# Kernel optimization log

Hardware: AMD Instinct MI355X
Metric: run time of the kernel (lower is better)

The kernel has to match this reference:

```python
import jax, jax.numpy as jnp
import numpy as np

H = 8          # num_attention_heads
HEAD_DIM = 24  # 192 / 8


def setup_inputs() -> dict:
    key = jax.random.key(0)
    k1, k2, k3 = jax.random.split(key, 3)
    B, S, D = 4, 2048, 192
    x = jax.random.normal(k1, (B, S, D), dtype=jnp.float32)
    mask0 = jnp.zeros((B, 1, 1, S), dtype=jnp.float32)  # HF additive attention mask
    w_attn = jax.random.normal(k2, (D, 3 * D), dtype=jnp.float32) * 0.02
    b_attn = jnp.zeros((3 * D,), dtype=jnp.float32)
    w_proj = jax.random.normal(k3, (D, D), dtype=jnp.float32) * 0.02
    b_proj = jnp.zeros((D,), dtype=jnp.float32)
    return {"x": x, "mask0": mask0, "w_attn": w_attn, "b_attn": b_attn,
            "w_proj": w_proj, "b_proj": b_proj}


def reference(x, mask0, w_attn, b_attn, w_proj, b_proj):
    B, S, D = x.shape
    # fused QKV projection (GPT2 Conv1D: x @ W + b)
    qkv = x @ w_attn + b_attn                       # [B,S,3D]
    q, k, v = jnp.split(qkv, 3, axis=-1)
    def split_heads(t):
        return t.reshape(B, S, H, HEAD_DIM).transpose(0, 2, 1, 3)  # [B,H,S,hd]
    q, k, v = split_heads(q), split_heads(k), split_heads(v)
    # scaled QK^T
    scores = jnp.einsum('bhqd,bhkd->bhqk', q, k) / jnp.sqrt(
        jnp.asarray(HEAD_DIM, dtype=q.dtype))
    # causal mask (masked_fill with dtype min), then additive padding mask
    causal = jnp.tril(jnp.ones((S, S), dtype=bool))
    mask_value = jnp.finfo(scores.dtype).min
    scores = jnp.where(causal, scores, mask_value) + mask0
    attn = jax.nn.softmax(scores, axis=-1)          # [B,H,S,S]
    # attn_dropout is identity in eval mode
    out = jnp.einsum('bhqk,bhkd->bhqd', attn, v)    # [B,H,S,hd]
    out = out.transpose(0, 2, 1, 3).reshape(B, S, D)
    return out @ w_proj + b_proj
```

## Files before the change

### kernel.cpp

```cpp
#include <hip/hip_runtime.h>

typedef unsigned short u16;
typedef unsigned int u32;
typedef __bf16 bf16x8 __attribute__((ext_vector_type(8)));
typedef float f32x4 __attribute__((ext_vector_type(4)));
typedef float f32x16 __attribute__((ext_vector_type(16)));
typedef u32 u32x2 __attribute__((ext_vector_type(2)));
typedef u32 u32x4 __attribute__((ext_vector_type(4)));

#define NB 4
#define NS 2048
#define ND 192
#define NH 8
#define HD 24
#define NM (NB*NS)
#define N3 (3*ND)
#define NBH (NB*NH)

#define LOG2E 1.4426950408889634f
#define QSCALE (0.20412414523193152f * 1.4426950408889634f)

__device__ __forceinline__ u16 f2bf(float f){
  union { float f; unsigned u; } a; a.f = f;
  unsigned r = a.u + 0x7fffu + ((a.u >> 16) & 1u);
  return (u16)(r >> 16);
}
__device__ __forceinline__ u32 cvtpk(float lo, float hi){
  u32 r; asm("v_cvt_pk_bf16_f32 %0, %1, %2" : "=v"(r) : "v"(lo), "v"(hi)); return r;
}
__device__ __forceinline__ void pswap(u32 &a, u32 &b){
  asm("v_permlane32_swap_b32 %0, %1" : "+v"(a), "+v"(b));
}

__device__ __forceinline__ void transpose64(
    const float* __restrict__ src, int srcN, u16* __restrict__ dst, int dstK,
    int k0, int n0, u16 (*sh)[68], int tid)
{
  int r = tid >> 2, cs = tid & 3;
  const float* sp = src + (size_t)(k0 + r)*srcN + n0 + cs*16;
  #pragma unroll
  for (int q = 0; q < 4; ++q) {
    float4 v = *(const float4*)(sp + q*4);
    u16 o[4] = { f2bf(v.x), f2bf(v.y), f2bf(v.z), f2bf(v.w) };
    *(u32x2*)&sh[r][cs*16 + q*4] = *(const u32x2*)o;
  }
  __syncthreads();
  int n = tid >> 2, ks = tid & 3;
  u16 tmp[16];
  #pragma unroll
  for (int j = 0; j < 16; ++j) tmp[j] = sh[ks*16 + j][n];
  u16* dp = dst + (size_t)(n0 + n)*dstK + k0 + ks*16;
  *(u32x4*)dp       = *(const u32x4*)tmp;
  *(u32x4*)(dp + 8) = *(const u32x4*)(tmp + 8);
}

__global__ __launch_bounds__(256) void prep_kernel(
    const float* __restrict__ x, const float* __restrict__ w_attn,
    const float* __restrict__ w_proj,
    u16* __restrict__ xb, u16* __restrict__ wta, u16* __restrict__ wtp)
{
  __shared__ u16 sh[64][68];
  const int bid = blockIdx.x, tid = threadIdx.x;
  if (bid < 1536) {
    int i = bid*256 + tid;
    float4 v = reinterpret_cast<const float4*>(x)[i];
    u16 o[4] = { f2bf(v.x), f2bf(v.y), f2bf(v.z), f2bf(v.w) };
    *reinterpret_cast<u32x2*>(xb + (size_t)i*4) = *(const u32x2*)o;
  } else if (bid < 1536 + 27) {
    int t = bid - 1536; int kt = t/9, nt = t%9;
    transpose64(w_attn, N3, wta, ND, kt*64, nt*64, sh, tid);
  } else {
    int t = bid - 1563; int kt = t/3, nt = t%3;
    transpose64(w_proj, ND, wtp, ND, kt*64, nt*64, sh, tid);
  }
}

__global__ __launch_bounds__(256) void qkv_kernel(
    const u16* __restrict__ xb, const u16* __restrict__ wta,
    const float* __restrict__ b_attn, const float* __restrict__ mask0,
    u16* __restrict__ qp, u16* __restrict__ kp, u16* __restrict__ vtp)
{
  __shared__ u16 tile[96*72];
  const int m0 = blockIdx.x*64, n0 = blockIdx.y*96;
  const int tid = threadIdx.x;
  const int w = tid >> 6, lane = tid & 63, c = lane & 15, g = lane >> 4;
  f32x4 acc[6] = {};
  const int ar = m0 + w*16 + c;
  #pragma unroll
  for (int ks = 0; ks < 6; ++ks) {
    bf16x8 af = *(const bf16x8*)(xb + (size_t)ar*ND + ks*32 + g*8);
    #pragma unroll
    for (int t = 0; t < 6; ++t) {
      bf16x8 bfr = *(const bf16x8*)(wta + (size_t)(n0 + t*16 + c)*ND + ks*32 + g*8);
      acc[t] = __builtin_amdgcn_mfma_f32_16x16x32_bf16(af, bfr, acc[t], 0, 0, 0);
    }
  }
  const int b = m0 >> 11, sb = m0 & (NS-1);
  if (n0 >= 384) {
    const int h0 = (n0 - 384)/HD;
    #pragma unroll
    for (int t = 0; t < 6; ++t) {
      float bias = b_attn[n0 + t*16 + c];
      #pragma unroll
      for (int r = 0; r < 4; ++r)
        tile[(t*16 + c)*72 + w*16 + g*4 + r] = f2bf(acc[t][r] + bias);
    }
    __syncthreads();
    if (tid < 200) {
      int row = tid >> 1, seg = tid & 1;
      if (row < 96) {
        int hl = row / HD, dv = row % HD;
        u16* dst = vtp + ((size_t)((b*NH + h0 + hl)*32 + dv))*NS + sb + seg*32;
        const u16* src = &tile[row*72 + seg*32];
        #pragma unroll
        for (int q = 0; q < 4; ++q)
          *(u32x4*)(dst + q*8) = *(const u32x4*)(src + q*8);
      } else {
        int hl = row - 96;
        u16* dst = vtp + ((size_t)((b*NH + h0 + hl)*32 + 24))*NS + sb + seg*32;
        u16 ones[8] = {0x3F80,0x3F80,0x3F80,0x3F80,0x3F80,0x3F80,0x3F80,0x3F80};
        #pragma unroll
        for (int q = 0; q < 4; ++q)
          *(u32x4*)(dst + q*8) = *(const u32x4*)ones;
      }
    }
  } else {
    const bool isQ = (n0 < 192);
    const float scl = isQ ? QSCALE : 1.0f;
    #pragma unroll
    for (int t = 0; t < 6; ++t) {
      float bias = b_attn[n0 + t*16 + c];
      #pragma unroll
      for (int r = 0; r < 4; ++r)
        tile[(w*16 + g*4 + r)*104 + t*16 + c] = f2bf((acc[t][r] + bias)*scl);
    }
    __syncthreads();
    int row = tid >> 2, run = tid & 3;
    int h0 = (n0 % 192)/HD;
    u16 d24 = isQ ? (u16)0x3F80
                  : f2bf(mask0[b*NS + sb + row] * LOG2E);
    const u16* src = &tile[row*104 + run*24];
    union { u32x4 q[4]; u16 s[32]; } buf;
    buf.q[0] = *(const u32x4*)(src);
    buf.q[1] = *(const u32x4*)(src + 8);
    buf.q[2] = *(const u32x4*)(src + 16);
    buf.s[24] = d24;
    #pragma unroll
    for (int j = 25; j < 32; ++j) buf.s[j] = 0;
    u16* dst = (isQ ? qp : kp)
             + ((size_t)((b*NS + sb + row)*NH + h0 + run))*32;
    #pragma unroll
    for (int q = 0; q < 4; ++q)
      *(u32x4*)(dst + q*8) = buf.q[q];
  }
}

__global__ __launch_bounds__(256) void attn_kernel(
    const u16* __restrict__ qp, const u16* __restrict__ kp,
    const u16* __restrict__ vtp, u16* __restrict__ ao)
{
  __shared__ u16 klds[2][64][40];
  __shared__ u16 vlds[2][32][72];
  u16 (*ot)[32][40] = (u16(*)[32][40])klds;

  const int bh = blockIdx.x;
  const int g  = 15 - (int)blockIdx.y;
  const int b = bh >> 3, h = bh & 7;
  const int tid = threadIdx.x;
  const int w = tid >> 6, lane = tid & 63, c = lane & 31, hi = lane >> 5;
  const int q0 = g*128 + w*32;
  const int nt = 2*g + 2;

  const size_t rowstride = NH*32;
  const size_t qkbase = (size_t)b*NS*rowstride + h*32;

  const u16* qrow = qp + qkbase + (size_t)(q0 + c)*rowstride;
  bf16x8 qf0 = *(const bf16x8*)(qrow + hi*8);
  bf16x8 qf1 = *(const bf16x8*)(qrow + 16 + hi*8);

  const int krow = tid >> 2, kch = tid & 3;
  const int vrow = tid >> 3, vch = tid & 7;
  const u16* kgsrc = kp + qkbase + (size_t)krow*rowstride + kch*8;
  const u16* vgsrc = vtp + ((size_t)(bh*32 + vrow))*NS + vch*8;

  u32x4 kreg = *(const u32x4*)(kgsrc);
  u32x4 vreg = *(const u32x4*)(vgsrc);
  *(u32x4*)&klds[0][krow][kch*8] = kreg;
  *(u32x4*)&vlds[0][vrow][vch*8] = vreg;
  __syncthreads();

  f32x16 o = {0};
  const f32x16 z16 = {0};
  float m = 0.f;

  for (int t = 0; t < nt; ++t) {
    const int cur = t & 1;
    if (t + 1 < nt) {
      kreg = *(const u32x4*)(kgsrc + (size_t)(t+1)*64*rowstride);
      vreg = *(const u32x4*)(vgsrc + (t+1)*64);
    }
    const int kb0 = t*64;
    if (kb0 <= q0) {
      const bool a1 = (kb0 + 32 <= q0);
      bf16x8 ka0 = *(const bf16x8*)&klds[cur][c][hi*8];
      bf16x8 ka1 = *(const bf16x8*)&klds[cur][c][16 + hi*8];
      f32x16 st = __builtin_amdgcn_mfma_f32_32x32x16_bf16(ka0, qf0, z16, 0, 0, 0);
      st        = __builtin_amdgcn_mfma_f32_32x32x16_bf16(ka1, qf1, st,  0, 0, 0);
      f32x16 su;
      if (a1) {
        bf16x8 kb0f = *(const bf16x8*)&klds[cur][32 + c][hi*8];
        bf16x8 kb1f = *(const bf16x8*)&klds[cur][32 + c][16 + hi*8];
        su = __builtin_amdgcn_mfma_f32_32x32x16_bf16(kb0f, qf0, z16, 0, 0, 0);
        su = __builtin_amdgcn_mfma_f32_32x32x16_bf16(kb1f, qf1, su,  0, 0, 0);
      }
      float pm = -3.0e38f;
      if (kb0 == q0) {
        #pragma unroll
        for (int r = 0; r < 16; ++r) {
          int krel = (r & 3) + 8*(r >> 2) + 4*hi;
          float s = (krel > c) ? -3.0e38f : st[r];
          st[r] = s; pm = fmaxf(pm, s);
        }
      } else {
        #pragma unroll
        for (int r = 0; r < 16; ++r) pm = fmaxf(pm, st[r]);
      }
      if (a1) {
        if (kb0 + 32 == q0) {
          #pragma unroll
          for (int r = 0; r < 16; ++r) {
            int krel = (r & 3) + 8*(r >> 2) + 4*hi;
            float s = (krel > c) ? -3.0e38f : su[r];
            su[r] = s; pm = fmaxf(pm, s);
          }
        } else {
          #pragma unroll
          for (int r = 0; r < 16; ++r) pm = fmaxf(pm, su[r]);
        }
      }
      if (!__all(pm - m <= 8.f)) {
        float pm2 = fmaxf(pm, __shfl_xor(pm, 32));
        float mn = fmaxf(m, pm2);
        float al = __builtin_amdgcn_exp2f(m - mn);
        #pragma unroll
        for (int r = 0; r < 16; ++r) o[r] *= al;
        m = mn;
      }
      #pragma unroll
      for (int r = 0; r < 16; ++r) st[r] = __builtin_amdgcn_exp2f(st[r] - m);
      if (a1) {
        #pragma unroll
        for (int r = 0; r < 16; ++r) su[r] = __builtin_amdgcn_exp2f(su[r] - m);
      }
      {
        u32 a0 = cvtpk(st[0], st[1]),  b0 = cvtpk(st[4], st[5]);
        u32 a1w = cvtpk(st[2], st[3]), b1 = cvtpk(st[6], st[7]);
        pswap(a0, b0); pswap(a1w, b1);
        u32 a2 = cvtpk(st[8], st[9]),  b2 = cvtpk(st[12], st[13]);
        u32 a3 = cvtpk(st[10], st[11]), b3 = cvtpk(st[14], st[15]);
        pswap(a2, b2); pswap(a3, b3);
        union { u32 wrd[4]; bf16x8 v; } pf0, pf1;
        pf0.wrd[0] = a0; pf0.wrd[1] = a1w; pf0.wrd[2] = b0; pf0.wrd[3] = b1;
        pf1.wrd[0] = a2; pf1.wrd[1] = a3;  pf1.wrd[2] = b2; pf1.wrd[3] = b3;
        bf16x8 va0 = *(const bf16x8*)&vlds[cur][c][hi*8];
        bf16x8 va1 = *(const bf16x8*)&vlds[cur][c][16 + hi*8];
        o = __builtin_amdgcn_mfma_f32_32x32x16_bf16(va0, pf0.v, o, 0, 0, 0);
        o = __builtin_amdgcn_mfma_f32_32x32x16_bf16(va1, pf1.v, o, 0, 0, 0);
      }
      if (a1) {
        u32 a0 = cvtpk(su[0], su[1]),  b0 = cvtpk(su[4], su[5]);
        u32 a1w = cvtpk(su[2], su[3]), b1 = cvtpk(su[6], su[7]);
        pswap(a0, b0); pswap(a1w, b1);
        u32 a2 = cvtpk(su[8], su[9]),  b2 = cvtpk(su[12], su[13]);
        u32 a3 = cvtpk(su[10], su[11]), b3 = cvtpk(su[14], su[15]);
        pswap(a2, b2); pswap(a3, b3);
        union { u32 wrd[4]; bf16x8 v; } pf0, pf1;
        pf0.wrd[0] = a0; pf0.wrd[1] = a1w; pf0.wrd[2] = b0; pf0.wrd[3] = b1;
        pf1.wrd[0] = a2; pf1.wrd[1] = a3;  pf1.wrd[2] = b2; pf1.wrd[3] = b3;
        bf16x8 va0 = *(const bf16x8*)&vlds[cur][c][32 + hi*8];
        bf16x8 va1 = *(const bf16x8*)&vlds[cur][c][48 + hi*8];
        o = __builtin_amdgcn_mfma_f32_32x32x16_bf16(va0, pf0.v, o, 0, 0, 0);
        o = __builtin_amdgcn_mfma_f32_32x32x16_bf16(va1, pf1.v, o, 0, 0, 0);
      }
    }
    if (t + 1 < nt) {
      *(u32x4*)&klds[cur^1][krow][kch*8] = kreg;
      *(u32x4*)&vlds[cur^1][vrow][vch*8] = vreg;
    }
    __syncthreads();
  }

  float lv = o[12];
  float lo_ = __shfl_xor(lv, 32);
  float l = hi ? lo_ : lv;
  float inv = 1.0f / l;
  #pragma unroll
  for (int r = 0; r < 12; ++r) {
    int d = (r & 3) + 8*(r >> 2) + 4*hi;
    ot[w][c][d] = f2bf(o[r]*inv);
  }
  int q = lane >> 1, half = lane & 1;
  const u16* src = &ot[w][q][half*12];
  u32x2 w0 = *(const u32x2*)src;
  u32x2 w1 = *(const u32x2*)(src + 4);
  u32x2 w2 = *(const u32x2*)(src + 8);
  u16* dst = ao + ((size_t)(b*NS + q0 + q))*ND + h*HD + half*12;
  *(u32x2*)dst       = w0;
  *(u32x2*)(dst + 4) = w1;
  *(u32x2*)(dst + 8) = w2;
}

__global__ __launch_bounds__(256) void proj_kernel(
    const u16* __restrict__ ao, const u16* __restrict__ wtp,
    const float* __restrict__ bp, float* __restrict__ out)
{
  const int m0 = blockIdx.x*64, n0 = blockIdx.y*64;
  const int tid = threadIdx.x;
  const int w = tid >> 6, lane = tid & 63, c = lane & 15, g = lane >> 4;
  f32x4 acc[4] = {};
  const int ar = m0 + w*16 + c;
  #pragma unroll
  for (int ks = 0; ks < 6; ++ks) {
    bf16x8 af = *(const bf16x8*)(ao + (size_t)ar*ND + ks*32 + g*8);
    #pragma unroll
    for (int t = 0; t < 4; ++t) {
      bf16x8 bfr = *(const bf16x8*)(wtp + (size_t)(n0 + t*16 + c)*ND + ks*32 + g*8);
      acc[t] = __builtin_amdgcn_mfma_f32_16x16x32_bf16(af, bfr, acc[t], 0, 0, 0);
    }
  }
  #pragma unroll
  for (int t = 0; t < 4; ++t) {
    int n = n0 + t*16 + c;
    float bias = bp[n];
    #pragma unroll
    for (int r = 0; r < 4; ++r) {
      int mm = m0 + w*16 + g*4 + r;
      out[(size_t)mm*ND + n] = acc[t][r] + bias;
    }
  }
}

extern "C" void kernel_launch(void* const* d_in, const int* in_sizes, int n_in,
                              void* d_out, int out_size, void* d_ws, size_t ws_size,
                              hipStream_t stream)
{
  const float* x      = (const float*)d_in[0];
  const float* mask0  = (const float*)d_in[1];
  const float* w_attn = (const float*)d_in[2];
  const float* b_attn = (const float*)d_in[3];
  const float* w_proj = (const float*)d_in[4];
  const float* b_proj = (const float*)d_in[5];
  float* out = (float*)d_out;

  char* ws = (char*)d_ws;
  u16* qp  = (u16*)(ws);
  u16* kp  = (u16*)(ws + ((size_t)4  << 20));
  u16* vtp = (u16*)(ws + ((size_t)8  << 20));
  u16* xb  = (u16*)(ws + ((size_t)12 << 20));
  u16* wta = (u16*)(ws + ((size_t)15 << 20));
  u16* wtp = (u16*)(ws + ((size_t)15 << 20) + 256*1024);
  u16* ao  = (u16*)(ws + ((size_t)15 << 20) + 512*1024);

  prep_kernel<<<1572, 256, 0, stream>>>(x, w_attn, w_proj, xb, wta, wtp);
  qkv_kernel<<<dim3(NM/64, 6), 256, 0, stream>>>(xb, wta, b_attn, mask0,
                                                 qp, kp, vtp);
  attn_kernel<<<dim3(NBH, 16), 256, 0, stream>>>(qp, kp, vtp, ao);
  proj_kernel<<<dim3(NM/64, ND/64), 256, 0, stream>>>(ao, wtp, b_proj, out);
}
```

Before: 139.3 us.

## Split attention KV range across two blocks with merge kernel; fuse x conversion into QKV

```diff
diff --git a/kernel.cpp b/kernel.cpp
--- a/kernel.cpp
+++ b/kernel.cpp
@@ -16,6 +16,7 @@
 #define NM (NB*NS)
 #define N3 (3*ND)
 #define NBH (NB*NH)
+#define NROWS (NBH*NS)
 
 #define LOG2E 1.4426950408889634f
 #define QSCALE (0.20412414523193152f * 1.4426950408889634f)
@@ -25,6 +26,9 @@
   unsigned r = a.u + 0x7fffu + ((a.u >> 16) & 1u);
   return (u16)(r >> 16);
 }
+__device__ __forceinline__ float b2f(u16 h){
+  union { u32 u; float f; } a; a.u = ((u32)h) << 16; return a.f;
+}
 __device__ __forceinline__ u32 cvtpk(float lo, float hi){
   u32 r; asm("v_cvt_pk_bf16_f32 %0, %1, %2" : "=v"(r) : "v"(lo), "v"(hi)); return r;
 }
@@ -55,28 +59,22 @@
 }
 
 __global__ __launch_bounds__(256) void prep_kernel(
-    const float* __restrict__ x, const float* __restrict__ w_attn,
-    const float* __restrict__ w_proj,
-    u16* __restrict__ xb, u16* __restrict__ wta, u16* __restrict__ wtp)
+    const float* __restrict__ w_attn, const float* __restrict__ w_proj,
+    u16* __restrict__ wta, u16* __restrict__ wtp)
 {
   __shared__ u16 sh[64][68];
   const int bid = blockIdx.x, tid = threadIdx.x;
-  if (bid < 1536) {
-    int i = bid*256 + tid;
-    float4 v = reinterpret_cast<const float4*>(x)[i];
-    u16 o[4] = { f2bf(v.x), f2bf(v.y), f2bf(v.z), f2bf(v.w) };
-    *reinterpret_cast<u32x2*>(xb + (size_t)i*4) = *(const u32x2*)o;
-  } else if (bid < 1536 + 27) {
-    int t = bid - 1536; int kt = t/9, nt = t%9;
+  if (bid < 27) {
+    int kt = bid/9, nt = bid%9;
     transpose64(w_attn, N3, wta, ND, kt*64, nt*64, sh, tid);
   } else {
-    int t = bid - 1563; int kt = t/3, nt = t%3;
+    int t = bid - 27; int kt = t/3, nt = t%3;
     transpose64(w_proj, ND, wtp, ND, kt*64, nt*64, sh, tid);
   }
 }
 
 __global__ __launch_bounds__(256) void qkv_kernel(
-    const u16* __restrict__ xb, const u16* __restrict__ wta,
+    const float* __restrict__ x, const u16* __restrict__ wta,
     const float* __restrict__ b_attn, const float* __restrict__ mask0,
     u16* __restrict__ qp, u16* __restrict__ kp, u16* __restrict__ vtp)
 {
@@ -86,9 +84,15 @@
   const int w = tid >> 6, lane = tid & 63, c = lane & 15, g = lane >> 4;
   f32x4 acc[6] = {};
   const int ar = m0 + w*16 + c;
+  const float* xrow = x + (size_t)ar*ND;
   #pragma unroll
   for (int ks = 0; ks < 6; ++ks) {
-    bf16x8 af = *(const bf16x8*)(xb + (size_t)ar*ND + ks*32 + g*8);
+    float4 xa = *(const float4*)(xrow + ks*32 + g*8);
+    float4 xc = *(const float4*)(xrow + ks*32 + g*8 + 4);
+    union { u32 wrd[4]; bf16x8 v; } afu;
+    afu.wrd[0] = cvtpk(xa.x, xa.y); afu.wrd[1] = cvtpk(xa.z, xa.w);
+    afu.wrd[2] = cvtpk(xc.x, xc.y); afu.wrd[3] = cvtpk(xc.z, xc.w);
+    bf16x8 af = afu.v;
     #pragma unroll
     for (int t = 0; t < 6; ++t) {
       bf16x8 bfr = *(const bf16x8*)(wta + (size_t)(n0 + t*16 + c)*ND + ks*32 + g*8);
@@ -157,19 +161,20 @@
 
 __global__ __launch_bounds__(256) void attn_kernel(
     const u16* __restrict__ qp, const u16* __restrict__ kp,
-    const u16* __restrict__ vtp, u16* __restrict__ ao)
+    const u16* __restrict__ vtp, u16* __restrict__ po, float* __restrict__ pmf)
 {
   __shared__ u16 klds[2][64][40];
   __shared__ u16 vlds[2][32][72];
-  u16 (*ot)[32][40] = (u16(*)[32][40])klds;
 
   const int bh = blockIdx.x;
   const int g  = 15 - (int)blockIdx.y;
+  const int part = blockIdx.z;
   const int b = bh >> 3, h = bh & 7;
   const int tid = threadIdx.x;
   const int w = tid >> 6, lane = tid & 63, c = lane & 31, hi = lane >> 5;
   const int q0 = g*128 + w*32;
-  const int nt = 2*g + 2;
+  const int t0 = part ? g + 1 : 0;
+  const int ntp = g + 1;
 
   const size_t rowstride = NH*32;
   const size_t qkbase = (size_t)b*NS*rowstride + h*32;
@@ -180,8 +185,8 @@
 
   const int krow = tid >> 2, kch = tid & 3;
   const int vrow = tid >> 3, vch = tid & 7;
-  const u16* kgsrc = kp + qkbase + (size_t)krow*rowstride + kch*8;
-  const u16* vgsrc = vtp + ((size_t)(bh*32 + vrow))*NS + vch*8;
+  const u16* kgsrc = kp + qkbase + (size_t)(t0*64 + krow)*rowstride + kch*8;
+  const u16* vgsrc = vtp + ((size_t)(bh*32 + vrow))*NS + t0*64 + vch*8;
 
   u32x4 kreg = *(const u32x4*)(kgsrc);
   u32x4 vreg = *(const u32x4*)(vgsrc);
@@ -193,25 +198,29 @@
   const f32x16 z16 = {0};
   float m = 0.f;
 
-  for (int t = 0; t < nt; ++t) {
-    const int cur = t & 1;
-    if (t + 1 < nt) {
-      kreg = *(const u32x4*)(kgsrc + (size_t)(t+1)*64*rowstride);
-      vreg = *(const u32x4*)(vgsrc + (t+1)*64);
-    }
-    const int kb0 = t*64;
+  for (int dt = 0; dt < ntp; ++dt) {
+    const int cur = dt & 1;
+    if (dt + 1 < ntp) {
+      kreg = *(const u32x4*)(kgsrc + (size_t)(dt+1)*64*rowstride);
+      vreg = *(const u32x4*)(vgsrc + (dt+1)*64);
+    }
+    const int kb0 = (t0 + dt)*64;
     if (kb0 <= q0) {
       const bool a1 = (kb0 + 32 <= q0);
       bf16x8 ka0 = *(const bf16x8*)&klds[cur][c][hi*8];
       bf16x8 ka1 = *(const bf16x8*)&klds[cur][c][16 + hi*8];
+      __builtin_amdgcn_s_setprio(1);
       f32x16 st = __builtin_amdgcn_mfma_f32_32x32x16_bf16(ka0, qf0, z16, 0, 0, 0);
       st        = __builtin_amdgcn_mfma_f32_32x32x16_bf16(ka1, qf1, st,  0, 0, 0);
+      __builtin_amdgcn_s_setprio(0);
       f32x16 su;
       if (a1) {
         bf16x8 kb0f = *(const bf16x8*)&klds[cur][32 + c][hi*8];
         bf16x8 kb1f = *(const bf16x8*)&klds[cur][32 + c][16 + hi*8];
+        __builtin_amdgcn_s_setprio(1);
         su = __builtin_amdgcn_mfma_f32_32x32x16_bf16(kb0f, qf0, z16, 0, 0, 0);
         su = __builtin_amdgcn_mfma_f32_32x32x16_bf16(kb1f, qf1, su,  0, 0, 0);
+        __builtin_amdgcn_s_setprio(0);
       }
       float pm = -3.0e38f;
       if (kb0 == q0) {
@@ -264,8 +273,10 @@
         pf1.wrd[0] = a2; pf1.wrd[1] = a3;  pf1.wrd[2] = b2; pf1.wrd[3] = b3;
         bf16x8 va0 = *(const bf16x8*)&vlds[cur][c][hi*8];
         bf16x8 va1 = *(const bf16x8*)&vlds[cur][c][16 + hi*8];
+        __builtin_amdgcn_s_setprio(1);
         o = __builtin_amdgcn_mfma_f32_32x32x16_bf16(va0, pf0.v, o, 0, 0, 0);
         o = __builtin_amdgcn_mfma_f32_32x32x16_bf16(va1, pf1.v, o, 0, 0, 0);
+        __builtin_amdgcn_s_setprio(0);
       }
       if (a1) {
         u32 a0 = cvtpk(su[0], su[1]),  b0 = cvtpk(su[4], su[5]);
@@ -279,35 +290,60 @@
         pf1.wrd[0] = a2; pf1.wrd[1] = a3;  pf1.wrd[2] = b2; pf1.wrd[3] = b3;
         bf16x8 va0 = *(const bf16x8*)&vlds[cur][c][32 + hi*8];
         bf16x8 va1 = *(const bf16x8*)&vlds[cur][c][48 + hi*8];
+        __builtin_amdgcn_s_setprio(1);
         o = __builtin_amdgcn_mfma_f32_32x32x16_bf16(va0, pf0.v, o, 0, 0, 0);
         o = __builtin_amdgcn_mfma_f32_32x32x16_bf16(va1, pf1.v, o, 0, 0, 0);
-      }
-    }
-    if (t + 1 < nt) {
+        __builtin_amdgcn_s_setprio(0);
+      }
+    }
+    if (dt + 1 < ntp) {
       *(u32x4*)&klds[cur^1][krow][kch*8] = kreg;
       *(u32x4*)&vlds[cur^1][vrow][vch*8] = vreg;
     }
     __syncthreads();
   }
 
-  float lv = o[12];
-  float lo_ = __shfl_xor(lv, 32);
-  float l = hi ? lo_ : lv;
+  const int pidx = part*NROWS + bh*NS + q0 + c;
+  u16* porow = po + (size_t)pidx*32;
+  #pragma unroll
+  for (int rr = 0; rr < 4; ++rr) {
+    u32 lo = cvtpk(o[rr*4 + 0], o[rr*4 + 1]);
+    u32 h2 = cvtpk(o[rr*4 + 2], o[rr*4 + 3]);
+    u32x2 wv = {lo, h2};
+    *(u32x2*)(porow + rr*8 + hi*4) = wv;
+  }
+  if (hi == 0) pmf[pidx] = (t0*64 <= q0) ? m : -3.0e38f;
+}
+
+__global__ __launch_bounds__(256) void merge_kernel(
+    const u16* __restrict__ po, const float* __restrict__ pmf,
+    u16* __restrict__ ao)
+{
+  int i = blockIdx.x*256 + threadIdx.x;
+  int bh = i >> 11, q = i & (NS-1);
+  int b = bh >> 3, h = bh & 7;
+  float m1 = pmf[i], m2 = pmf[NROWS + i];
+  float M = fmaxf(m1, m2);
+  float w1 = __builtin_amdgcn_exp2f(m1 - M);
+  float w2 = __builtin_amdgcn_exp2f(m2 - M);
+  const u16* r1 = po + (size_t)i*32;
+  const u16* r2 = r1 + (size_t)NROWS*32;
+  u16 a1[32], a2[32];
+  #pragma unroll
+  for (int q4 = 0; q4 < 4; ++q4) {
+    *(u32x4*)(a1 + q4*8) = *(const u32x4*)(r1 + q4*8);
+    *(u32x4*)(a2 + q4*8) = *(const u32x4*)(r2 + q4*8);
+  }
+  float l = b2f(a1[24])*w1 + b2f(a2[24])*w2;
   float inv = 1.0f / l;
-  #pragma unroll
-  for (int r = 0; r < 12; ++r) {
-    int d = (r & 3) + 8*(r >> 2) + 4*hi;
-    ot[w][c][d] = f2bf(o[r]*inv);
-  }
-  int q = lane >> 1, half = lane & 1;
-  const u16* src = &ot[w][q][half*12];
-  u32x2 w0 = *(const u32x2*)src;
-  u32x2 w1 = *(const u32x2*)(src + 4);
-  u32x2 w2 = *(const u32x2*)(src + 8);
-  u16* dst = ao + ((size_t)(b*NS + q0 + q))*ND + h*HD + half*12;
-  *(u32x2*)dst       = w0;
-  *(u32x2*)(dst + 4) = w1;
-  *(u32x2*)(dst + 8) = w2;
+  u16 ob[24];
+  #pragma unroll
+  for (int d = 0; d < 24; ++d)
+    ob[d] = f2bf((b2f(a1[d])*w1 + b2f(a2[d])*w2)*inv);
+  u16* dst = ao + ((size_t)(b*NS + q))*ND + h*HD;
+  #pragma unroll
+  for (int q4 = 0; q4 < 3; ++q4)
+    *(u32x4*)(dst + q4*8) = *(const u32x4*)(ob + q4*8);
 }
 
 __global__ __launch_bounds__(256) void proj_kernel(
@@ -353,17 +389,19 @@
   float* out = (float*)d_out;
 
   char* ws = (char*)d_ws;
-  u16* qp  = (u16*)(ws);
-  u16* kp  = (u16*)(ws + ((size_t)4  << 20));
-  u16* vtp = (u16*)(ws + ((size_t)8  << 20));
-  u16* xb  = (u16*)(ws + ((size_t)12 << 20));
-  u16* wta = (u16*)(ws + ((size_t)15 << 20));
-  u16* wtp = (u16*)(ws + ((size_t)15 << 20) + 256*1024);
-  u16* ao  = (u16*)(ws + ((size_t)15 << 20) + 512*1024);
-
-  prep_kernel<<<1572, 256, 0, stream>>>(x, w_attn, w_proj, xb, wta, wtp);
-  qkv_kernel<<<dim3(NM/64, 6), 256, 0, stream>>>(xb, wta, b_attn, mask0,
+  u16*   qp  = (u16*)(ws);
+  u16*   kp  = (u16*)(ws + ((size_t)4  << 20));
+  u16*   vtp = (u16*)(ws + ((size_t)8  << 20));
+  u16*   wta = (u16*)(ws + ((size_t)12 << 20));
+  u16*   wtp = (u16*)(ws + ((size_t)12 << 20) + 256*1024);
+  u16*   ao  = (u16*)(ws + ((size_t)12 << 20) + 512*1024);
+  u16*   po  = (u16*)(ws + ((size_t)16 << 20));
+  float* pmf = (float*)(ws + ((size_t)24 << 20));
+
+  prep_kernel<<<36, 256, 0, stream>>>(w_attn, w_proj, wta, wtp);
+  qkv_kernel<<<dim3(NM/64, 6), 256, 0, stream>>>(x, wta, b_attn, mask0,
                                                  qp, kp, vtp);
-  attn_kernel<<<dim3(NBH, 16), 256, 0, stream>>>(qp, kp, vtp, ao);
+  attn_kernel<<<dim3(NBH, 16, 2), 256, 0, stream>>>(qp, kp, vtp, po, pmf);
+  merge_kernel<<<256, 256, 0, stream>>>(po, pmf, ao);
   proj_kernel<<<dim3(NM/64, ND/64), 256, 0, stream>>>(ao, wtp, b_proj, out);
 }
```

Result: faster. 133.9 us (-3.9%).
